# Optimization experiments

Measured on AMD Instinct MI355X. Metric: run time of the kernel, lower is better.

Reference implementation:

```python
import jax, jax.numpy as jnp
import numpy as np

E, T = 8, 256          # n_experts, chunk length
IN, OUT = 1024, 1024   # input_size, output_size
D1, D2 = 32, 32        # nearest factors of IN
DO1, DO2 = 32, 32      # nearest factors of OUT
B, L = 8, 2048
LOSS_COEF = 1e-5


def setup_inputs() -> dict:
    key = jax.random.key(0)
    ks = jax.random.split(key, 12)
    eyeE = lambda d, k: (jnp.broadcast_to(jnp.eye(d, dtype=jnp.float32), (E, d, d))
                         + 0.01 * jax.random.normal(k, (E, d, d), jnp.float32))
    return {
        "x": jax.random.normal(ks[0], (B, L, IN), jnp.float32),
        "w_gate": 0.02 * jax.random.normal(ks[1], (IN, E), jnp.float32),
        "weight": 0.02 * jax.random.normal(ks[2], (E, OUT, IN), jnp.float32),
        "bias": 0.02 * jax.random.normal(ks[3], (E, OUT), jnp.float32),
        "res_weight": 0.02 * jax.random.normal(ks[4], (OUT, IN), jnp.float32),
        "res_bias": 0.02 * jax.random.normal(ks[5], (1, OUT), jnp.float32),
        "curve1_in": eyeE(D1, ks[6]),
        "curve2_in": eyeE(D2, ks[7]),
        "curve1_out": eyeE(DO1, ks[8]),
        "curve2_out": eyeE(DO2, ks[9]),
        "curve1_bias": eyeE(DO1, ks[10]),
        "curve2_bias": eyeE(DO2, ks[11]),
    }


def _cv_squared(v):
    v = v.astype(jnp.float32)
    return jnp.var(v, ddof=1) / (jnp.mean(v) ** 2 + 1e-10)


def reference(x, w_gate, weight, bias, res_weight, res_bias,
              curve1_in, curve2_in, curve1_out, curve2_out,
              curve1_bias, curve2_bias):
    Bx, Lx, d = x.shape
    N = Lx // T
    BN = Bx * N
    xr = x.reshape(BN, T, d)

    # --- gating (eval mode, ties_merging forces k = n_experts -> plain softmax) ---
    logits = xr.mean(axis=1) @ w_gate            # [BN, E]
    gates = jax.nn.softmax(logits, axis=1)        # [BN, E]
    load = (gates > 0).sum(axis=0).astype(jnp.float32)
    importance = gates.sum(axis=0)
    loss = (_cv_squared(importance) + _cv_squared(load)) * LOSS_COEF

    # --- roll gates by one segment, keeping each sample's first chunk (detached) ---
    e_first = jax.lax.stop_gradient(gates.reshape(Bx, N, E)[:, 0])
    g = jnp.roll(gates, 1, axis=0).reshape(Bx, N, E)
    g = g.at[:, 0].set(e_first).reshape(BN, E)

    # --- Kronecker curve-factored expert weight merge ---
    rw = (weight - res_weight).reshape(E, DO1, DO2, D1, D2)
    rw = jnp.einsum('bij,bjklm->biklm', curve1_out, rw)
    rw = jnp.einsum('bik,bjklm->bjilm', curve2_out, rw)
    rw = jnp.einsum('bil,bjklm->bjkim', curve1_in, rw)
    rw = jnp.einsum('bim,bjklm->bjkli', curve2_in, rw)
    rw = rw.reshape(E, OUT, IN)
    expert_weights = res_weight + jnp.einsum('be,eoi->boi', g, rw)  # [BN, O, I]

    y = jnp.einsum('bij,bkj->bik', xr, expert_weights)  # [BN, T, O]

    # --- curve-factored expert bias merge ---
    rb = (bias - res_bias).reshape(E, DO1, DO2)
    rb = jnp.einsum('bki,bij->bkj', curve1_bias, rb)      # [E, DO1, DO2]
    rb = jnp.einsum('bkj,bij->bik', curve2_bias, rb)      # [E, DO1, DO2]
    rb = rb.reshape(E, OUT)
    expert_bias = res_bias + jnp.einsum('be,eo->bo', g, rb)  # [BN, O]

    y = (y + expert_bias[:, None, :]).reshape(Bx, Lx, OUT)
    return y, loss
```

## Files before the change

kernel.cpp:

```cpp
#include <hip/hip_runtime.h>
#include <cstdint>

typedef __bf16 bf16x8 __attribute__((ext_vector_type(8)));
typedef float  f32x4  __attribute__((ext_vector_type(4)));
using u16 = unsigned short;

struct alignas(8) u16x4 { u16 x, y, z, w; };

__device__ __forceinline__ u16 f2bf(float f) {
  unsigned u = __builtin_bit_cast(unsigned, f);
  u = (u + 0x7FFFu + ((u >> 16) & 1u)) >> 16;
  return (u16)u;
}
__device__ __forceinline__ float bf2f(u16 u) {
  unsigned v = ((unsigned)u) << 16;
  return __builtin_bit_cast(float, v);
}

#define ASYNC16(gp, lp) __builtin_amdgcn_global_load_lds( \
    (__attribute__((address_space(1))) void*)(void*)(gp),  \
    (__attribute__((address_space(3))) void*)(lp), 16, 0, 0)

static constexpr size_t OFF_XBF  = 0;
static constexpr size_t OFF_EW   = 33554432;
static constexpr size_t OFF_T2   = 33554432;
static constexpr size_t OFF_PM   = 67108864;
static constexpr size_t OFF_RW   = 167772160;
static constexpr size_t OFF_LG   = 201326592;
static constexpr size_t OFF_G    = 201588736;
static constexpr size_t OFF_RB   = 201592832;
static constexpr size_t OFF_EB   = 201625600;
static constexpr size_t WS_NEED  = 201887744;

__global__ __launch_bounds__(256) void k_means(const float* __restrict__ x,
                                               float* __restrict__ pm,
                                               u16* __restrict__ xbf) {
  int b = blockIdx.x, q = blockIdx.y, tid = threadIdx.x;
  const float* xb = x + (size_t)b * 262144 + (size_t)q * 16384 + tid * 4;
  u16* xo = xbf + (size_t)b * 262144 + (size_t)q * 16384 + tid * 4;
  float s0 = 0.f, s1 = 0.f, s2 = 0.f, s3 = 0.f;
#pragma unroll
  for (int t = 0; t < 16; ++t) {
    float4 v = *(const float4*)(xb + t * 1024);
    s0 += v.x; s1 += v.y; s2 += v.z; s3 += v.w;
    u16x4 o; o.x = f2bf(v.x); o.y = f2bf(v.y); o.z = f2bf(v.z); o.w = f2bf(v.w);
    *(u16x4*)(xo + t * 1024) = o;
  }
  float4 sv; sv.x = s0; sv.y = s1; sv.z = s2; sv.w = s3;
  *(float4*)(pm + ((size_t)b * 16 + q) * 1024 + tid * 4) = sv;
}

__global__ __launch_bounds__(256) void k_redlogits(const float* __restrict__ pm,
                                                   const float* __restrict__ w_gate,
                                                   float* __restrict__ logits) {
  __shared__ float red[4][8];
  int b = blockIdx.x, tid = threadIdx.x;
  const float* p = pm + (size_t)b * 16384 + tid * 4;
  float4 s = {0.f, 0.f, 0.f, 0.f};
#pragma unroll
  for (int q = 0; q < 16; ++q) {
    float4 v = *(const float4*)(p + q * 1024);
    s.x += v.x; s.y += v.y; s.z += v.z; s.w += v.w;
  }
  int i0 = tid * 4;
  float acc[8];
#pragma unroll
  for (int e = 0; e < 8; ++e) {
    acc[e] = s.x * w_gate[(i0 + 0) * 8 + e] + s.y * w_gate[(i0 + 1) * 8 + e]
           + s.z * w_gate[(i0 + 2) * 8 + e] + s.w * w_gate[(i0 + 3) * 8 + e];
  }
#pragma unroll
  for (int off = 32; off >= 1; off >>= 1)
#pragma unroll
    for (int e = 0; e < 8; ++e) acc[e] += __shfl_down(acc[e], off, 64);
  int wv = tid >> 6;
  if ((tid & 63) == 0)
#pragma unroll
    for (int e = 0; e < 8; ++e) red[wv][e] = acc[e];
  __syncthreads();
  if (tid < 8)
    logits[b * 8 + tid] =
        (red[0][tid] + red[1][tid] + red[2][tid] + red[3][tid]) * (1.f / 256.f);
}

__global__ __launch_bounds__(64) void k_gatefin(const float* __restrict__ logits,
                                                float* __restrict__ g,
                                                float* __restrict__ loss_out) {
  __shared__ float gates[64][8];
  __shared__ float imp[8];
  int b = threadIdx.x;
  {
    float lg[8];
#pragma unroll
    for (int j = 0; j < 8; ++j) lg[j] = logits[b * 8 + j];
    float mx = lg[0];
#pragma unroll
    for (int j = 1; j < 8; ++j) mx = fmaxf(mx, lg[j]);
    float s = 0.f, ex[8];
#pragma unroll
    for (int j = 0; j < 8; ++j) { ex[j] = expf(lg[j] - mx); s += ex[j]; }
    float inv = 1.f / s;
#pragma unroll
    for (int j = 0; j < 8; ++j) gates[b][j] = ex[j] * inv;
  }
  __syncthreads();
  if (b < 8) {
    float s = 0.f;
    for (int bb = 0; bb < 64; ++bb) s += gates[bb][b];
    imp[b] = s;
  }
  __syncthreads();
  if (b == 0) {
    float mean = 0.f;
#pragma unroll
    for (int j = 0; j < 8; ++j) mean += imp[j];
    mean *= (1.f / 8.f);
    float var = 0.f;
#pragma unroll
    for (int j = 0; j < 8; ++j) { float d = imp[j] - mean; var += d * d; }
    var *= (1.f / 7.f);
    loss_out[0] = (var / (mean * mean + 1e-10f)) * 1e-5f;
  }
  __syncthreads();
  {
    int src = ((b & 7) == 0) ? b : b - 1;
#pragma unroll
    for (int j = 0; j < 8; ++j) g[b * 8 + j] = gates[src][j];
  }
}

__global__ __launch_bounds__(256) void k_mergeA(const float* __restrict__ W,
                                                const float* __restrict__ R,
                                                const float* __restrict__ c1o,
                                                const float* __restrict__ c2o,
                                                float* __restrict__ T2t) {
  __shared__ float dw[8 * 1024];
  __shared__ float m1[1024], m2[1024];
  int e = blockIdx.y, c0 = blockIdx.x * 8, tid = threadIdx.x;
  const float* We = W + (size_t)e * 1048576;
  for (int idx = tid; idx < 1024; idx += 256) {
    m1[idx] = c1o[e * 1024 + idx];
    m2[idx] = c2o[e * 1024 + idx];
  }
  {
    int r = tid >> 1, h = (tid & 1) * 4;
#pragma unroll
    for (int i = 0; i < 8; ++i) {
      int row = r + i * 128;
      const float4 wv = *(const float4*)(We + (size_t)row * 1024 + c0 + h);
      const float4 rv = *(const float4*)(R + (size_t)row * 1024 + c0 + h);
      dw[(h + 0) * 1024 + row] = wv.x - rv.x;
      dw[(h + 1) * 1024 + row] = wv.y - rv.y;
      dw[(h + 2) * 1024 + row] = wv.z - rv.z;
      dw[(h + 3) * 1024 + row] = wv.w - rv.w;
    }
  }
  __syncthreads();
  int i1 = tid & 31, c = tid >> 5;
  const float* dwc = dw + c * 1024;
  float U[32];
#pragma unroll
  for (int k = 0; k < 32; ++k) U[k] = 0.f;
  for (int j = 0; j < 32; ++j) {
    float cj = m1[i1 * 32 + j];
    const float4* rowp = (const float4*)(dwc + j * 32);
#pragma unroll
    for (int k4 = 0; k4 < 8; ++k4) {
      float4 v = rowp[k4];
      U[k4 * 4 + 0] += cj * v.x; U[k4 * 4 + 1] += cj * v.y;
      U[k4 * 4 + 2] += cj * v.z; U[k4 * 4 + 3] += cj * v.w;
    }
  }
  float* obase = T2t + (size_t)e * 1048576 + (size_t)(c0 + c) * 1024 + i1 * 32;
#pragma unroll
  for (int g4 = 0; g4 < 8; ++g4) {
    float s[4];
#pragma unroll
    for (int q = 0; q < 4; ++q) {
      const float4* m2r = (const float4*)(m2 + (g4 * 4 + q) * 32);
      float acc = 0.f;
#pragma unroll
      for (int k4 = 0; k4 < 8; ++k4) {
        float4 mv = m2r[k4];
        acc += mv.x * U[k4 * 4 + 0] + mv.y * U[k4 * 4 + 1]
             + mv.z * U[k4 * 4 + 2] + mv.w * U[k4 * 4 + 3];
      }
      s[q] = acc;
    }
    float4 o4; o4.x = s[0]; o4.y = s[1]; o4.z = s[2]; o4.w = s[3];
    *(float4*)(obase + g4 * 4) = o4;
  }
}

__global__ __launch_bounds__(256) void k_mergeB(const float* __restrict__ T2t,
                                                const float* __restrict__ c1i,
                                                const float* __restrict__ c2i,
                                                u16* __restrict__ RWbf) {
  __shared__ float t2[8 * 1024];
  __shared__ float m1[1024], m2[1024];
  int e = blockIdx.y, o0 = blockIdx.x * 8, tid = threadIdx.x;
  const float* Te = T2t + (size_t)e * 1048576;
  for (int idx = tid; idx < 1024; idx += 256) {
    m1[idx] = c1i[e * 1024 + idx];
    m2[idx] = c2i[e * 1024 + idx];
  }
  {
    int r = tid >> 1, h = (tid & 1) * 4;
#pragma unroll
    for (int i = 0; i < 8; ++i) {
      int row = r + i * 128;
      const float4 tv = *(const float4*)(Te + (size_t)row * 1024 + o0 + h);
      t2[(h + 0) * 1024 + row] = tv.x;
      t2[(h + 1) * 1024 + row] = tv.y;
      t2[(h + 2) * 1024 + row] = tv.z;
      t2[(h + 3) * 1024 + row] = tv.w;
    }
  }
  __syncthreads();
  int i1 = tid & 31, oc = tid >> 5;
  const float* t2c = t2 + oc * 1024;
  float A[32];
#pragma unroll
  for (int m = 0; m < 32; ++m) A[m] = 0.f;
  for (int l = 0; l < 32; ++l) {
    float cl = m1[i1 * 32 + l];
    const float4* rowp = (const float4*)(t2c + l * 32);
#pragma unroll
    for (int m4 = 0; m4 < 8; ++m4) {
      float4 v = rowp[m4];
      A[m4 * 4 + 0] += cl * v.x; A[m4 * 4 + 1] += cl * v.y;
      A[m4 * 4 + 2] += cl * v.z; A[m4 * 4 + 3] += cl * v.w;
    }
  }
  u16* obase = RWbf + ((size_t)e * 1024 + o0 + oc) * 1024 + i1 * 32;
#pragma unroll
  for (int g4 = 0; g4 < 8; ++g4) {
    float s[4];
#pragma unroll
    for (int q = 0; q < 4; ++q) {
      const float4* m2r = (const float4*)(m2 + (g4 * 4 + q) * 32);
      float acc = 0.f;
#pragma unroll
      for (int m4 = 0; m4 < 8; ++m4) {
        float4 mv = m2r[m4];
        acc += mv.x * A[m4 * 4 + 0] + mv.y * A[m4 * 4 + 1]
             + mv.z * A[m4 * 4 + 2] + mv.w * A[m4 * 4 + 3];
      }
      s[q] = acc;
    }
    u16x4 o4; o4.x = f2bf(s[0]); o4.y = f2bf(s[1]); o4.z = f2bf(s[2]); o4.w = f2bf(s[3]);
    *(u16x4*)(obase + g4 * 4) = o4;
  }
}

__global__ __launch_bounds__(256) void k_rb(const float* __restrict__ bias,
                                            const float* __restrict__ res_bias,
                                            const float* __restrict__ c1b,
                                            const float* __restrict__ c2b,
                                            float* __restrict__ rb) {
  __shared__ float rb0[32][33], rb1[32][33], m1[32][32], m2[32][32];
  int e = blockIdx.x, tid = threadIdx.x;
  for (int idx = tid; idx < 1024; idx += 256) {
    int i = idx >> 5, j = idx & 31;
    rb0[i][j] = bias[e * 1024 + idx] - res_bias[idx];
    m1[i][j] = c1b[e * 1024 + idx];
    m2[i][j] = c2b[e * 1024 + idx];
  }
  __syncthreads();
  for (int idx = tid; idx < 1024; idx += 256) {
    int p = idx >> 5, j = idx & 31;
    float s = 0.f;
#pragma unroll
    for (int i = 0; i < 32; ++i) s += m1[p][i] * rb0[i][j];
    rb1[p][j] = s;
  }
  __syncthreads();
  for (int idx = tid; idx < 1024; idx += 256) {
    int p = idx >> 5, q = idx & 31;
    float s = 0.f;
#pragma unroll
    for (int j = 0; j < 32; ++j) s += m2[q][j] * rb1[p][j];
    rb[e * 1024 + idx] = s;
  }
}

__global__ __launch_bounds__(256) void k_combine(const u16* __restrict__ RWbf,
                                                 const float* __restrict__ R,
                                                 const float* __restrict__ g,
                                                 u16* __restrict__ EW) {
  __shared__ float gs[512];
  int o = blockIdx.x, tid = threadIdx.x;
  for (int idx = tid; idx < 512; idx += 256) gs[idx] = g[idx];
  __syncthreads();
  int i0 = tid * 4;
  float4 r4 = *(const float4*)(R + (size_t)o * 1024 + i0);
  float4 w[8];
#pragma unroll
  for (int e = 0; e < 8; ++e) {
    u16x4 t = *(const u16x4*)(RWbf + (size_t)e * 1048576 + (size_t)o * 1024 + i0);
    w[e].x = bf2f(t.x); w[e].y = bf2f(t.y); w[e].z = bf2f(t.z); w[e].w = bf2f(t.w);
  }
  for (int b = 0; b < 64; ++b) {
    float a0 = r4.x, a1 = r4.y, a2 = r4.z, a3 = r4.w;
#pragma unroll
    for (int e = 0; e < 8; ++e) {
      float ge = gs[b * 8 + e];
      a0 += ge * w[e].x; a1 += ge * w[e].y; a2 += ge * w[e].z; a3 += ge * w[e].w;
    }
    u16x4 u; u.x = f2bf(a0); u.y = f2bf(a1); u.z = f2bf(a2); u.w = f2bf(a3);
    *(u16x4*)(EW + (size_t)b * 1048576 + (size_t)o * 1024 + i0) = u;
  }
}

__global__ __launch_bounds__(512) void k_gemm(const u16* __restrict__ Xb,
                                              const u16* __restrict__ EW,
                                              const float* __restrict__ rb,
                                              const float* __restrict__ res_b,
                                              const float* __restrict__ g,
                                              float* __restrict__ Y) {
  __shared__ alignas(16) u16 As[256 * 64];
  __shared__ alignas(16) u16 Bs[256 * 64];
  int hw = blockIdx.x;
  int xcd = hw & 7;
  int b  = xcd * 8 + (hw >> 5);
  int nt = (hw >> 3) & 3;
  int t0 = b * 256, o0 = nt * 256;
  int tid = threadIdx.x, lane = tid & 63, wv = tid >> 6;
  int wr = wv >> 2, wc = wv & 3;
  f32x4 acc[8][4] = {};
  const u16* aG = Xb + (size_t)t0 * 1024;
  const u16* bG = EW + (size_t)b * 1048576 + (size_t)o0 * 1024;
  int srow = tid >> 3;
  int scol = (tid & 7) << 3;
  int gcol = (((tid & 7) ^ (srow & 7)) << 3);
  int lr = lane & 15;
  int sx = lr & 7;
  for (int kt = 0; kt < 16; ++kt) {
    int k0 = kt << 6;
#pragma unroll
    for (int iss = 0; iss < 4; ++iss) {
      int r = srow + iss * 64;
      ASYNC16(aG + (size_t)r * 1024 + k0 + gcol, &As[r * 64 + scol]);
      ASYNC16(bG + (size_t)r * 1024 + k0 + gcol, &Bs[r * 64 + scol]);
    }
    __syncthreads();
#pragma unroll
    for (int kk = 0; kk < 2; ++kk) {
      int c16 = kk * 4 + (lane >> 4);
      int cp = ((c16 ^ sx) << 3);
      bf16x8 af[8], bfr[4];
#pragma unroll
      for (int mi = 0; mi < 8; ++mi)
        af[mi] = *(const bf16x8*)&As[(wr * 128 + mi * 16 + lr) * 64 + cp];
#pragma unroll
      for (int ni = 0; ni < 4; ++ni)
        bfr[ni] = *(const bf16x8*)&Bs[(wc * 64 + ni * 16 + lr) * 64 + cp];
#pragma unroll
      for (int mi = 0; mi < 8; ++mi)
#pragma unroll
        for (int ni = 0; ni < 4; ++ni)
          acc[mi][ni] = __builtin_amdgcn_mfma_f32_16x16x32_bf16(af[mi], bfr[ni], acc[mi][ni], 0, 0, 0);
    }
    __syncthreads();
  }
  float ge[8];
#pragma unroll
  for (int e = 0; e < 8; ++e) ge[e] = g[b * 8 + e];
  int rbase = (lane >> 4) << 2;
#pragma unroll
  for (int ni = 0; ni < 4; ++ni) {
    int o = o0 + wc * 64 + ni * 16 + lr;
    float ebv = res_b[o];
#pragma unroll
    for (int e = 0; e < 8; ++e) ebv += ge[e] * rb[e * 1024 + o];
#pragma unroll
    for (int mi = 0; mi < 8; ++mi) {
      int trow = t0 + wr * 128 + mi * 16 + rbase;
      float* yp = Y + (size_t)trow * 1024 + o;
      yp[0]    = acc[mi][ni][0] + ebv;
      yp[1024] = acc[mi][ni][1] + ebv;
      yp[2048] = acc[mi][ni][2] + ebv;
      yp[3072] = acc[mi][ni][3] + ebv;
    }
  }
}

extern "C" void kernel_launch(void* const* d_in, const int* in_sizes, int n_in,
                              void* d_out, int out_size, void* d_ws, size_t ws_size,
                              hipStream_t stream) {
  const float* x      = (const float*)d_in[0];
  const float* w_gate = (const float*)d_in[1];
  const float* weight = (const float*)d_in[2];
  const float* bias   = (const float*)d_in[3];
  const float* res_w  = (const float*)d_in[4];
  const float* res_b  = (const float*)d_in[5];
  const float* c1i    = (const float*)d_in[6];
  const float* c2i    = (const float*)d_in[7];
  const float* c1o    = (const float*)d_in[8];
  const float* c2o    = (const float*)d_in[9];
  const float* c1b    = (const float*)d_in[10];
  const float* c2b    = (const float*)d_in[11];
  float* y = (float*)d_out;

  if (ws_size < WS_NEED) return;

  char* wsb = (char*)d_ws;
  u16*   xbf   = (u16*)(wsb + OFF_XBF);
  u16*   EW    = (u16*)(wsb + OFF_EW);
  float* T2t   = (float*)(wsb + OFF_T2);
  float* pm    = (float*)(wsb + OFF_PM);
  u16*   RWbf  = (u16*)(wsb + OFF_RW);
  float* lgts  = (float*)(wsb + OFF_LG);
  float* g     = (float*)(wsb + OFF_G);
  float* rb    = (float*)(wsb + OFF_RB);

  k_means    <<<dim3(64, 16), 256, 0, stream>>>(x, pm, xbf);
  k_redlogits<<<64, 256, 0, stream>>>(pm, w_gate, lgts);
  k_gatefin  <<<1, 64, 0, stream>>>(lgts, g, y + 16777216);
  k_mergeA   <<<dim3(128, 8), 256, 0, stream>>>(weight, res_w, c1o, c2o, T2t);
  k_mergeB   <<<dim3(128, 8), 256, 0, stream>>>(T2t, c1i, c2i, RWbf);
  k_rb       <<<8, 256, 0, stream>>>(bias, res_b, c1b, c2b, rb);
  k_combine  <<<1024, 256, 0, stream>>>(RWbf, res_w, g, EW);
  k_gemm     <<<256, 512, 0, stream>>>(xbf, EW, rb, res_b, g, y);
}
```

Before: 239.1 us.

## Double-buffer GEMM LDS tiles via register prefetch and store merge intermediate in bf16

The GEMM kernel replaces direct global-to-LDS async loads with register-staged prefetch of the next K tile into a second LDS buffer. This overlaps global loads with MFMA work and drops one barrier per iteration. The intermediate T2t tensor between the two merge kernels is also stored in bf16 instead of fp32, halving its write and read traffic. The costs are extra LDS (two 64 KB buffer pairs, which may cut occupancy), more register pressure, and some precision loss in the merge intermediate.

Measured after the change: 232.5 us. 1.03x faster.

```diff
diff --git a/kernel.cpp b/kernel.cpp
--- a/kernel.cpp
+++ b/kernel.cpp
@@ -3,6 +3,7 @@
 
 typedef __bf16 bf16x8 __attribute__((ext_vector_type(8)));
 typedef float  f32x4  __attribute__((ext_vector_type(4)));
+typedef unsigned int u32x4 __attribute__((ext_vector_type(4)));
 using u16 = unsigned short;
 
 struct alignas(8) u16x4 { u16 x, y, z, w; };
@@ -16,10 +17,6 @@
   unsigned v = ((unsigned)u) << 16;
   return __builtin_bit_cast(float, v);
 }
-
-#define ASYNC16(gp, lp) __builtin_amdgcn_global_load_lds( \
-    (__attribute__((address_space(1))) void*)(void*)(gp),  \
-    (__attribute__((address_space(3))) void*)(lp), 16, 0, 0)
 
 static constexpr size_t OFF_XBF  = 0;
 static constexpr size_t OFF_EW   = 33554432;
@@ -29,7 +26,6 @@
 static constexpr size_t OFF_LG   = 201326592;
 static constexpr size_t OFF_G    = 201588736;
 static constexpr size_t OFF_RB   = 201592832;
-static constexpr size_t OFF_EB   = 201625600;
 static constexpr size_t WS_NEED  = 201887744;
 
 __global__ __launch_bounds__(256) void k_means(const float* __restrict__ x,
@@ -133,7 +129,7 @@
                                                 const float* __restrict__ R,
                                                 const float* __restrict__ c1o,
                                                 const float* __restrict__ c2o,
-                                                float* __restrict__ T2t) {
+                                                u16* __restrict__ T2t) {
   __shared__ float dw[8 * 1024];
   __shared__ float m1[1024], m2[1024];
   int e = blockIdx.y, c0 = blockIdx.x * 8, tid = threadIdx.x;
@@ -171,7 +167,7 @@
       U[k4 * 4 + 2] += cj * v.z; U[k4 * 4 + 3] += cj * v.w;
     }
   }
-  float* obase = T2t + (size_t)e * 1048576 + (size_t)(c0 + c) * 1024 + i1 * 32;
+  u16* obase = T2t + (size_t)e * 1048576 + (size_t)(c0 + c) * 1024 + i1 * 32;
 #pragma unroll
   for (int g4 = 0; g4 < 8; ++g4) {
     float s[4];
@@ -187,19 +183,19 @@
       }
       s[q] = acc;
     }
-    float4 o4; o4.x = s[0]; o4.y = s[1]; o4.z = s[2]; o4.w = s[3];
-    *(float4*)(obase + g4 * 4) = o4;
-  }
-}
-
-__global__ __launch_bounds__(256) void k_mergeB(const float* __restrict__ T2t,
+    u16x4 o4; o4.x = f2bf(s[0]); o4.y = f2bf(s[1]); o4.z = f2bf(s[2]); o4.w = f2bf(s[3]);
+    *(u16x4*)(obase + g4 * 4) = o4;
+  }
+}
+
+__global__ __launch_bounds__(256) void k_mergeB(const u16* __restrict__ T2t,
                                                 const float* __restrict__ c1i,
                                                 const float* __restrict__ c2i,
                                                 u16* __restrict__ RWbf) {
   __shared__ float t2[8 * 1024];
   __shared__ float m1[1024], m2[1024];
   int e = blockIdx.y, o0 = blockIdx.x * 8, tid = threadIdx.x;
-  const float* Te = T2t + (size_t)e * 1048576;
+  const u16* Te = T2t + (size_t)e * 1048576;
   for (int idx = tid; idx < 1024; idx += 256) {
     m1[idx] = c1i[e * 1024 + idx];
     m2[idx] = c2i[e * 1024 + idx];
@@ -209,11 +205,11 @@
 #pragma unroll
     for (int i = 0; i < 8; ++i) {
       int row = r + i * 128;
-      const float4 tv = *(const float4*)(Te + (size_t)row * 1024 + o0 + h);
-      t2[(h + 0) * 1024 + row] = tv.x;
-      t2[(h + 1) * 1024 + row] = tv.y;
-      t2[(h + 2) * 1024 + row] = tv.z;
-      t2[(h + 3) * 1024 + row] = tv.w;
+      const u16x4 tv = *(const u16x4*)(Te + (size_t)row * 1024 + o0 + h);
+      t2[(h + 0) * 1024 + row] = bf2f(tv.x);
+      t2[(h + 1) * 1024 + row] = bf2f(tv.y);
+      t2[(h + 2) * 1024 + row] = bf2f(tv.z);
+      t2[(h + 3) * 1024 + row] = bf2f(tv.w);
     }
   }
   __syncthreads();
@@ -318,8 +314,8 @@
                                               const float* __restrict__ res_b,
                                               const float* __restrict__ g,
                                               float* __restrict__ Y) {
-  __shared__ alignas(16) u16 As[256 * 64];
-  __shared__ alignas(16) u16 Bs[256 * 64];
+  __shared__ alignas(16) u16 As[2][256 * 64];
+  __shared__ alignas(16) u16 Bs[2][256 * 64];
   int hw = blockIdx.x;
   int xcd = hw & 7;
   int b  = xcd * 8 + (hw >> 5);
@@ -331,19 +327,35 @@
   const u16* aG = Xb + (size_t)t0 * 1024;
   const u16* bG = EW + (size_t)b * 1048576 + (size_t)o0 * 1024;
   int srow = tid >> 3;
-  int scol = (tid & 7) << 3;
-  int gcol = (((tid & 7) ^ (srow & 7)) << 3);
+  int kcol = (tid & 7) << 3;
   int lr = lane & 15;
   int sx = lr & 7;
+  u32x4 la[4], lb[4];
+#pragma unroll
+  for (int iss = 0; iss < 4; ++iss) {
+    int r = srow + iss * 64;
+    la[iss] = *(const u32x4*)(aG + (size_t)r * 1024 + kcol);
+    lb[iss] = *(const u32x4*)(bG + (size_t)r * 1024 + kcol);
+  }
   for (int kt = 0; kt < 16; ++kt) {
-    int k0 = kt << 6;
+    int cur = kt & 1;
 #pragma unroll
     for (int iss = 0; iss < 4; ++iss) {
       int r = srow + iss * 64;
-      ASYNC16(aG + (size_t)r * 1024 + k0 + gcol, &As[r * 64 + scol]);
-      ASYNC16(bG + (size_t)r * 1024 + k0 + gcol, &Bs[r * 64 + scol]);
+      int wcl = (((tid & 7) ^ (r & 7)) << 3);
+      *(u32x4*)&As[cur][r * 64 + wcl] = la[iss];
+      *(u32x4*)&Bs[cur][r * 64 + wcl] = lb[iss];
     }
     __syncthreads();
+    if (kt < 15) {
+      int k0n = (kt + 1) << 6;
+#pragma unroll
+      for (int iss = 0; iss < 4; ++iss) {
+        int r = srow + iss * 64;
+        la[iss] = *(const u32x4*)(aG + (size_t)r * 1024 + k0n + kcol);
+        lb[iss] = *(const u32x4*)(bG + (size_t)r * 1024 + k0n + kcol);
+      }
+    }
 #pragma unroll
     for (int kk = 0; kk < 2; ++kk) {
       int c16 = kk * 4 + (lane >> 4);
@@ -351,17 +363,16 @@
       bf16x8 af[8], bfr[4];
 #pragma unroll
       for (int mi = 0; mi < 8; ++mi)
-        af[mi] = *(const bf16x8*)&As[(wr * 128 + mi * 16 + lr) * 64 + cp];
+        af[mi] = *(const bf16x8*)&As[cur][(wr * 128 + mi * 16 + lr) * 64 + cp];
 #pragma unroll
       for (int ni = 0; ni < 4; ++ni)
-        bfr[ni] = *(const bf16x8*)&Bs[(wc * 64 + ni * 16 + lr) * 64 + cp];
+        bfr[ni] = *(const bf16x8*)&Bs[cur][(wc * 64 + ni * 16 + lr) * 64 + cp];
 #pragma unroll
       for (int mi = 0; mi < 8; ++mi)
 #pragma unroll
         for (int ni = 0; ni < 4; ++ni)
           acc[mi][ni] = __builtin_amdgcn_mfma_f32_16x16x32_bf16(af[mi], bfr[ni], acc[mi][ni], 0, 0, 0);
     }
-    __syncthreads();
   }
   float ge[8];
 #pragma unroll
@@ -407,7 +418,7 @@
   char* wsb = (char*)d_ws;
   u16*   xbf   = (u16*)(wsb + OFF_XBF);
   u16*   EW    = (u16*)(wsb + OFF_EW);
-  float* T2t   = (float*)(wsb + OFF_T2);
+  u16*   T2t   = (u16*)(wsb + OFF_T2);
   float* pm    = (float*)(wsb + OFF_PM);
   u16*   RWbf  = (u16*)(wsb + OFF_RW);
   float* lgts  = (float*)(wsb + OFF_LG);
```
